# Optimization experiments

Measured on AMD Instinct MI355X. Metric: run time of the kernel, lower is better.

## Reference

```python
import jax, jax.numpy as jnp
import numpy as np

NUM_BATCH = 16  # B: number of point clouds in the ragged batch
NUM_POINTS = 500000  # N: total points across the batch
NUM_TRANS = 128  # M*B: stacked SE3 transforms (num_multi = 8)


def setup_inputs() -> dict:
    key = jax.random.key(0)
    k1, k2, k3 = jax.random.split(key, 3)
    trans = jax.random.normal(k1, (NUM_TRANS, 4, 4), dtype=jnp.float32)
    xyz = jax.random.normal(k2, (NUM_POINTS, 3), dtype=jnp.float32)
    batch = jax.random.randint(k3, (NUM_POINTS,), 0, NUM_BATCH, dtype=jnp.int32)
    # guarantee batch.max() + 1 == NUM_BATCH (matches the module's assert)
    batch = batch.at[:NUM_BATCH].set(jnp.arange(NUM_BATCH, dtype=jnp.int32))
    return {"trans": trans, "xyz": xyz, "batch": batch}


def reference(trans, xyz, batch):
    """SE3Transform.forward (PARTIAL_DENSE path) == multi_partial_transform.

    trans: [M*B, 4, 4], xyz: [N, 3], batch: [N] in [0, B).
    Returns (new_pos [M*N, 3], new_batch [M*N]).
    The original's per-batch Python loop with boolean masks is expressed as a
    single fused gather + per-point affine: out_i = R[nb_i] @ x_i + p[nb_i].
    """
    B = NUM_BATCH
    M = trans.shape[0] // B
    N = xyz.shape[0]
    # replicate points M times, offset batch ids per replica
    offs = (jnp.arange(M, dtype=batch.dtype) * B)[:, None]  # [M,1]
    new_batch = (batch[None, :] + offs).reshape(-1)  # [M*N]
    xyz_rep = jnp.broadcast_to(xyz[None], (M, N, 3)).reshape(-1, 3)  # [M*N,3]
    R = trans[new_batch, :3, :3]  # [M*N,3,3]
    p = trans[new_batch, :3, 3]   # [M*N,3]
    new_pos = jnp.einsum('nij,nj->ni', R, xyz_rep) + p
    return new_pos, new_batch
```

## Files before the change

### kernel.cpp

```cpp
#include <hip/hip_runtime.h>


#define N_POINTS 500000
#define N_BATCH  16
#define M_TRANS  8
#define NT       128
#define TSTRIDE  20

__global__ __launch_bounds__(256) void se3_kernel(
    const float* __restrict__ trans,
    const float* __restrict__ xyz,
    const int*   __restrict__ batch,
    float* __restrict__ out)
{
    __shared__ float s_trans[NT * TSTRIDE];

    for (int i = threadIdx.x; i < NT * 4; i += 256) {
        int pt  = i >> 2;
        int row = i & 3;
        float4 v = ((const float4*)trans)[i];
        *(float4*)&s_trans[pt * TSTRIDE + row * 4] = v;
    }
    __syncthreads();

    int g  = blockIdx.x * 256 + threadIdx.x;
    int n0 = g * 4;
    if (n0 >= N_POINTS) return;

    int4 b4 = ((const int4*)batch)[g];
    int bi[4] = {b4.x, b4.y, b4.z, b4.w};

    float4 x0 = ((const float4*)xyz)[g * 3 + 0];
    float4 x1 = ((const float4*)xyz)[g * 3 + 1];
    float4 x2 = ((const float4*)xyz)[g * 3 + 2];
    float px[4] = {x0.x, x0.w, x1.z, x2.y};
    float py[4] = {x0.y, x1.x, x1.w, x2.z};
    float pz[4] = {x0.z, x1.y, x2.x, x2.w};

    float* out_pos   = out;
    float* out_batch = out + 12000000;

    #pragma unroll
    for (int m = 0; m < M_TRANS; ++m) {
        float o[12];
        float nbf[4];
        #pragma unroll
        for (int j = 0; j < 4; ++j) {
            int nb = bi[j] + m * N_BATCH;
            nbf[j] = (float)nb;
            const float* T = &s_trans[nb * TSTRIDE];
            float4 r0 = *(const float4*)(T + 0);
            float4 r1 = *(const float4*)(T + 4);
            float4 r2 = *(const float4*)(T + 8);
            o[j * 3 + 0] = fmaf(r0.x, px[j], fmaf(r0.y, py[j], fmaf(r0.z, pz[j], r0.w)));
            o[j * 3 + 1] = fmaf(r1.x, px[j], fmaf(r1.y, py[j], fmaf(r1.z, pz[j], r1.w)));
            o[j * 3 + 2] = fmaf(r2.x, px[j], fmaf(r2.y, py[j], fmaf(r2.z, pz[j], r2.w)));
        }
        float* dst = out_pos + (size_t)m * (N_POINTS * 3) + (size_t)n0 * 3;
        ((float4*)dst)[0] = make_float4(o[0], o[1], o[2],  o[3]);
        ((float4*)dst)[1] = make_float4(o[4], o[5], o[6],  o[7]);
        ((float4*)dst)[2] = make_float4(o[8], o[9], o[10], o[11]);
        float* bdst = out_batch + (size_t)m * N_POINTS + n0;
        *(float4*)bdst = make_float4(nbf[0], nbf[1], nbf[2], nbf[3]);
    }
}

extern "C" void kernel_launch(void* const* d_in, const int* in_sizes, int n_in,
                              void* d_out, int out_size, void* d_ws, size_t ws_size,
                              hipStream_t stream) {
    const float* trans = (const float*)d_in[0];
    const float* xyz   = (const float*)d_in[1];
    const int*   batch = (const int*)d_in[2];
    float* out = (float*)d_out;

    const int groups = N_POINTS / 4;
    const int block  = 256;
    const int grid   = (groups + block - 1) / block;
    se3_kernel<<<grid, block, 0, stream>>>(trans, xyz, batch, out);
}
```

Before: 87.68 us.

## Map one thread per output float4 and split position and batch-id writes

Threads are remapped so each one produces a single float4 of the position output (spanning parts of two points) across all 8 replicas. Input xyz is staged through shared memory with a small halo. A separate set of threads writes the batch-id output from int4 loads. This raises parallelism roughly 4x and makes each store fully coalesced, at the cost of extra index arithmetic, shared-memory staging, and scalar batch loads.

Result: faster. 82.98 us (median of 2 runs) (-5.4%).

```diff
diff --git a/kernel.cpp b/kernel.cpp
--- a/kernel.cpp
+++ b/kernel.cpp
@@ -1,11 +1,11 @@
 #include <hip/hip_runtime.h>
 
 
-#define N_POINTS 500000
-#define N_BATCH  16
-#define M_TRANS  8
-#define NT       128
-#define TSTRIDE  20
+#define NPTS   500000
+#define POSF4  375000
+#define BATF4  125000
+#define NT     128
+#define TSTR   20
 
 __global__ __launch_bounds__(256) void se3_kernel(
     const float* __restrict__ trans,
@@ -13,55 +13,78 @@
     const int*   __restrict__ batch,
     float* __restrict__ out)
 {
-    __shared__ float s_trans[NT * TSTRIDE];
+    __shared__ float  s_t[NT * TSTR];
+    __shared__ float4 s_x[264];
 
-    for (int i = threadIdx.x; i < NT * 4; i += 256) {
-        int pt  = i >> 2;
-        int row = i & 3;
+    const int tid = threadIdx.x;
+    const int F   = blockIdx.x * 256;
+    const int t   = F + tid;
+
+    for (int i = tid; i < NT * 4; i += 256) {
+        int pt = i >> 2, row = i & 3;
         float4 v = ((const float4*)trans)[i];
-        *(float4*)&s_trans[pt * TSTRIDE + row * 4] = v;
+        *(float4*)&s_t[pt * TSTR + row * 4] = v;
+    }
+    if (F < POSF4) {
+        for (int i = tid; i < 264; i += 256) {
+            int idx = F - 2 + i;
+            idx = idx < 0 ? 0 : (idx >= POSF4 ? POSF4 - 1 : idx);
+            s_x[i] = ((const float4*)xyz)[idx];
+        }
     }
     __syncthreads();
 
-    int g  = blockIdx.x * 256 + threadIdx.x;
-    int n0 = g * 4;
-    if (n0 >= N_POINTS) return;
+    if (t < POSF4) {
+        const int f  = t;
+        const int t3 = f % 3;
+        const int n0 = (4 * f - t3) / 3;
 
-    int4 b4 = ((const int4*)batch)[g];
-    int bi[4] = {b4.x, b4.y, b4.z, b4.w};
+        const float* sxf = (const float*)s_x;
+        const int off = 4 * tid + 8 - t3;
+        float xa = sxf[off + 0], xb = sxf[off + 1], xc = sxf[off + 2];
+        float xd = sxf[off + 3], xe = sxf[off + 4], xf = sxf[off + 5];
 
-    float4 x0 = ((const float4*)xyz)[g * 3 + 0];
-    float4 x1 = ((const float4*)xyz)[g * 3 + 1];
-    float4 x2 = ((const float4*)xyz)[g * 3 + 2];
-    float px[4] = {x0.x, x0.w, x1.z, x2.y};
-    float py[4] = {x0.y, x1.x, x1.w, x2.z};
-    float pz[4] = {x0.z, x1.y, x2.x, x2.w};
+        const int b0 = batch[n0];
+        const int b1 = batch[n0 + 1];
 
-    float* out_pos   = out;
-    float* out_batch = out + 12000000;
+        int   ro[4];
+        float X0[4], X1[4], X2[4];
+        #pragma unroll
+        for (int k = 0; k < 4; ++k) {
+            int ck = t3 + k, sel = 0;
+            if (ck >= 3) { ck -= 3; sel = 1; }
+            int b = sel ? b1 : b0;
+            ro[k] = b * (TSTR * 4) + ck * 16;
+            X0[k] = sel ? xd : xa;
+            X1[k] = sel ? xe : xb;
+            X2[k] = sel ? xf : xc;
+        }
 
-    #pragma unroll
-    for (int m = 0; m < M_TRANS; ++m) {
-        float o[12];
-        float nbf[4];
+        const char* stb = (const char*)s_t;
+        float4* po = (float4*)out;
         #pragma unroll
-        for (int j = 0; j < 4; ++j) {
-            int nb = bi[j] + m * N_BATCH;
-            nbf[j] = (float)nb;
-            const float* T = &s_trans[nb * TSTRIDE];
-            float4 r0 = *(const float4*)(T + 0);
-            float4 r1 = *(const float4*)(T + 4);
-            float4 r2 = *(const float4*)(T + 8);
-            o[j * 3 + 0] = fmaf(r0.x, px[j], fmaf(r0.y, py[j], fmaf(r0.z, pz[j], r0.w)));
-            o[j * 3 + 1] = fmaf(r1.x, px[j], fmaf(r1.y, py[j], fmaf(r1.z, pz[j], r1.w)));
-            o[j * 3 + 2] = fmaf(r2.x, px[j], fmaf(r2.y, py[j], fmaf(r2.z, pz[j], r2.w)));
+        for (int m = 0; m < 8; ++m) {
+            float4 r0 = *(const float4*)(stb + ro[0] + m * 1280);
+            float4 r1 = *(const float4*)(stb + ro[1] + m * 1280);
+            float4 r2 = *(const float4*)(stb + ro[2] + m * 1280);
+            float4 r3 = *(const float4*)(stb + ro[3] + m * 1280);
+            float4 v;
+            v.x = fmaf(r0.x, X0[0], fmaf(r0.y, X1[0], fmaf(r0.z, X2[0], r0.w)));
+            v.y = fmaf(r1.x, X0[1], fmaf(r1.y, X1[1], fmaf(r1.z, X2[1], r1.w)));
+            v.z = fmaf(r2.x, X0[2], fmaf(r2.y, X1[2], fmaf(r2.z, X2[2], r2.w)));
+            v.w = fmaf(r3.x, X0[3], fmaf(r3.y, X1[3], fmaf(r3.z, X2[3], r3.w)));
+            po[m * POSF4 + f] = v;
         }
-        float* dst = out_pos + (size_t)m * (N_POINTS * 3) + (size_t)n0 * 3;
-        ((float4*)dst)[0] = make_float4(o[0], o[1], o[2],  o[3]);
-        ((float4*)dst)[1] = make_float4(o[4], o[5], o[6],  o[7]);
-        ((float4*)dst)[2] = make_float4(o[8], o[9], o[10], o[11]);
-        float* bdst = out_batch + (size_t)m * N_POINTS + n0;
-        *(float4*)bdst = make_float4(nbf[0], nbf[1], nbf[2], nbf[3]);
+    } else if (t < POSF4 + BATF4) {
+        const int q = t - POSF4;
+        int4 b4 = ((const int4*)batch)[q];
+        float4* ob = (float4*)(out + 12000000);
+        #pragma unroll
+        for (int m = 0; m < 8; ++m) {
+            const int a = m * 16;
+            ob[m * BATF4 + q] = make_float4((float)(b4.x + a), (float)(b4.y + a),
+                                            (float)(b4.z + a), (float)(b4.w + a));
+        }
     }
 }
 
@@ -73,8 +96,8 @@
     const int*   batch = (const int*)d_in[2];
     float* out = (float*)d_out;
 
-    const int groups = N_POINTS / 4;
-    const int block  = 256;
-    const int grid   = (groups + block - 1) / block;
+    const int total = POSF4 + BATF4;
+    const int block = 256;
+    const int grid  = (total + block - 1) / block;
     se3_kernel<<<grid, block, 0, stream>>>(trans, xyz, batch, out);
 }
```
